# Kernel optimization log

Measured on AMD Instinct MI355X. Metric: run time of the kernel, lower is better.

The kernel has to match this reference:

```python
import jax, jax.numpy as jnp
import numpy as np

N = 8192          # nodes in batch
D_IN = 512        # in_channels
G = 512           # global_dim
D_OUT = 512       # out_channels
H = 8             # heads
C = 2048          # num_centroids
NUM_NODES = 100000


def setup_inputs() -> dict:
    key = jax.random.key(0)
    ks = jax.random.split(key, 10)
    s = lambda fan_in: 1.0 / np.sqrt(fan_in)
    return {
        "x": jax.random.normal(ks[0], (N, D_IN), jnp.float32),
        "W_proj": jax.random.normal(ks[1], (D_IN, G), jnp.float32) * s(D_IN),
        "b_proj": jnp.zeros((G,), jnp.float32),
        "W_q": jax.random.normal(ks[2], (G, D_OUT), jnp.float32) * s(G),
        "b_q": jnp.zeros((D_OUT,), jnp.float32),
        "W_k": jax.random.normal(ks[3], (G, D_OUT), jnp.float32) * s(G),
        "b_k": jnp.zeros((D_OUT,), jnp.float32),
        "W_v": jax.random.normal(ks[4], (G, D_OUT), jnp.float32) * s(G),
        "b_v": jnp.zeros((D_OUT,), jnp.float32),
        "k_buf": jax.random.normal(ks[5], (C, G), jnp.float32),
        "v_buf": jax.random.normal(ks[6], (C, G), jnp.float32),
        "ln_gamma": jnp.ones((D_OUT,), jnp.float32),
        "ln_beta": jnp.zeros((D_OUT,), jnp.float32),
        "c_idx": jax.random.randint(ks[7], (NUM_NODES,), 0, C, jnp.int64 if jax.config.jax_enable_x64 else jnp.int32),
        "node_indices": jax.random.randint(ks[8], (N,), 0, NUM_NODES, jnp.int64 if jax.config.jax_enable_x64 else jnp.int32),
    }


def _layer_norm(y, gamma, beta, eps=1e-5):
    mu = jnp.mean(y, axis=-1, keepdims=True)
    var = jnp.var(y, axis=-1, keepdims=True)
    return (y - mu) * jax.lax.rsqrt(var + eps) * gamma + beta


def reference(x, W_proj, b_proj, W_q, b_q, W_k, b_k, W_v, b_v,
              k_buf, v_buf, ln_gamma, ln_beta, c_idx, node_indices):
    h, d = H, D_OUT
    dh = d // h
    scale = 1.0 / np.sqrt(d)  # source scales by 1/sqrt(out_channels)

    q_x = x @ W_proj + b_proj                      # [N, G]
    k_x = jax.lax.stop_gradient(k_buf)             # detach().clone()
    v_x = jax.lax.stop_gradient(v_buf)

    # n (h d) -> h n d
    q = (q_x @ W_q + b_q).reshape(-1, h, dh).transpose(1, 0, 2)   # [h, N, dh]
    k = (k_x @ W_k + b_k).reshape(-1, h, dh).transpose(1, 0, 2)   # [h, C, dh]
    v = (v_x @ W_v + b_v).reshape(-1, h, dh).transpose(1, 0, 2)   # [h, C, dh]

    dots = jnp.einsum('hnd,hcd->hnc', q, k) * scale               # [h, N, C]

    # log-count centroid bias (unique/bincount over the full c_idx buffer)
    counts = jnp.bincount(c_idx, length=C)                        # [C] int
    dots = dots + jnp.log(counts.astype(dots.dtype))              # log(0)=-inf masks empty centroids

    attn = jax.nn.softmax(dots, axis=-1)                          # [h, N, C]
    out = jnp.einsum('hnc,hcd->hnd', attn, v)                     # [h, N, dh]
    out = out.transpose(1, 0, 2).reshape(-1, d)                   # [N, d]

    return _layer_norm(out, ln_gamma, ln_beta)
```

## Files before the change

### kernel.cpp

```cpp
#include <hip/hip_runtime.h>
#include <math.h>

typedef __bf16 bf16x8 __attribute__((ext_vector_type(8)));
typedef __bf16 bf16x2 __attribute__((ext_vector_type(2)));
typedef float f32x4 __attribute__((ext_vector_type(4)));
typedef float f32x16 __attribute__((ext_vector_type(16)));
typedef unsigned u32x2v __attribute__((ext_vector_type(2)));
typedef unsigned short u16;

#define NQ 8192
#define DMODEL 512
#define NHEAD 8
#define DH 64
#define NC 2048
#define NIDX 100000

__device__ __forceinline__ u16 f2bf(float f) {
    unsigned u = __float_as_uint(f);
    u += 0x7fffu + ((u >> 16) & 1u);
    return (u16)(u >> 16);
}
__device__ __forceinline__ float bf2f(u16 h) {
    return __uint_as_float(((unsigned)h) << 16);
}
__device__ __forceinline__ unsigned pk2(float a, float b) {
    bf16x2 t; t[0] = (__bf16)a; t[1] = (__bf16)b;
    return __builtin_bit_cast(unsigned, t);
}
__device__ __forceinline__ void plswap(unsigned& a, unsigned& b) {
    u32x2v r = __builtin_amdgcn_permlane32_swap(a, b, false, false);
    a = r[0]; b = r[1];
}
__device__ __forceinline__ int soff(int q, int col) {
    return q * 256 + ((((col >> 2) ^ (q & 7)) << 2) | (col & 3));
}

__global__ __launch_bounds__(256) void k_prep2(
    const float* __restrict__ Wp, const float* __restrict__ Wq, const float* __restrict__ Wk,
    const float* __restrict__ Wv, const float* __restrict__ bp, const float* __restrict__ bq_,
    const int* __restrict__ cidx,
    u16* __restrict__ Wp_bf, u16* __restrict__ Wq_t, u16* __restrict__ Wk_t,
    u16* __restrict__ Wv_t, int* __restrict__ counts, float* __restrict__ bcomb)
{
    __shared__ float tile[32][33];
    int bid = blockIdx.x, tid = threadIdx.x;
    if (bid < 256) {
        int e = (bid * 256 + tid) * 4;
        float4 v = *(const float4*)(Wp + e);
        ushort4 o;
        o.x = f2bf(v.x); o.y = f2bf(v.y); o.z = f2bf(v.z); o.w = f2bf(v.w);
        *(ushort4*)(Wp_bf + e) = o;
    } else if (bid < 1024) {
        const float* W; u16* Wt; int tb;
        if (bid < 512)       { W = Wq; Wt = Wq_t; tb = bid - 256; }
        else if (bid < 768)  { W = Wk; Wt = Wk_t; tb = bid - 512; }
        else                 { W = Wv; Wt = Wv_t; tb = bid - 768; }
        int c0 = (tb & 15) * 32, r0 = (tb >> 4) * 32;
        int tx = tid & 31, ty = tid >> 5;
#pragma unroll
        for (int i = 0; i < 4; i++)
            tile[ty + i * 8][tx] = W[(size_t)(r0 + ty + i * 8) * DMODEL + c0 + tx];
        __syncthreads();
#pragma unroll
        for (int i = 0; i < 4; i++)
            Wt[(size_t)(c0 + ty + i * 8) * DMODEL + r0 + tx] = f2bf(tile[tx][ty + i * 8]);
    } else if (bid < 1152) {
        for (int i = (bid - 1024) * 256 + tid; i < NIDX; i += 128 * 256)
            atomicAdd(&counts[cidx[i]], 1);
    } else {
        int j = (bid - 1152) * 256 + tid;
        float s = bq_[j];
        for (int k = 0; k < DMODEL; k++) s += bp[k] * Wq[(size_t)k * DMODEL + j];
        bcomb[j] = s;
    }
}

template <int A_F32, int OUT_T>
__device__ __forceinline__ void gemm_bt_body(
    const void* __restrict__ A_, const u16* __restrict__ Bt,
    const float* __restrict__ bias, u16* __restrict__ Cmat,
    int M, int N, int K, int bx, int by)
{
    constexpr int LDP = 40;
    __shared__ __align__(16) u16 As[128 * LDP];
    __shared__ __align__(16) u16 Bs[128 * LDP];
    int tid = threadIdx.x;
    int lane = tid & 63, wid = tid >> 6;
    int wrow = (wid >> 1) * 64, wcol = (wid & 1) * 64;
    int m0 = by * 128, n0 = bx * 128;
    int lr = lane & 15, lg = lane >> 4;
    f32x4 acc[4][4] = {};

    for (int k0 = 0; k0 < K; k0 += 32) {
#pragma unroll
        for (int c = 0; c < 2; c++) {
            int ch = tid + c * 256;
            int row = ch >> 2, colc = (ch & 3) * 8;
            uint4 av;
            if (A_F32) {
                const float* Af = (const float*)A_;
                float4 a0 = *(const float4*)(Af + (size_t)(m0 + row) * K + k0 + colc);
                float4 a1 = *(const float4*)(Af + (size_t)(m0 + row) * K + k0 + colc + 4);
                av.x = pk2(a0.x, a0.y); av.y = pk2(a0.z, a0.w);
                av.z = pk2(a1.x, a1.y); av.w = pk2(a1.z, a1.w);
            } else {
                av = *(const uint4*)((const u16*)A_ + (size_t)(m0 + row) * K + k0 + colc);
            }
            *(uint4*)(&As[row * LDP + colc]) = av;
            uint4 bv = *(const uint4*)(Bt + (size_t)(n0 + row) * K + k0 + colc);
            *(uint4*)(&Bs[row * LDP + colc]) = bv;
        }
        __syncthreads();
        bf16x8 af[4], bfr[4];
#pragma unroll
        for (int m = 0; m < 4; m++)
            af[m] = *(const bf16x8*)(&As[(wrow + m * 16 + lr) * LDP + lg * 8]);
#pragma unroll
        for (int n = 0; n < 4; n++)
            bfr[n] = *(const bf16x8*)(&Bs[(wcol + n * 16 + lr) * LDP + lg * 8]);
#pragma unroll
        for (int m = 0; m < 4; m++)
#pragma unroll
            for (int n = 0; n < 4; n++)
                acc[m][n] = __builtin_amdgcn_mfma_f32_16x16x32_bf16(af[m], bfr[n], acc[m][n], 0, 0, 0);
        __syncthreads();
    }
#pragma unroll
    for (int n = 0; n < 4; n++) {
        int col = n0 + wcol + n * 16 + lr;
        float bv = bias ? bias[col] : 0.0f;
#pragma unroll
        for (int m = 0; m < 4; m++) {
            int rbase = m0 + wrow + m * 16 + lg * 4;
            if (OUT_T == 1) {
                int hh = col >> 6, T = (col >> 5) & 1, ql = col & 31;
                int t = rbase >> 5, cc = rbase & 31;
                int u = ((cc >> 4) * 2 + ((cc >> 3) & 1)) * 2 + T;
                size_t off = (size_t)hh * 131072 + (size_t)t * 2048 + u * 256 + ql * 8 + (cc & 7);
                ushort4 o4;
                o4.x = f2bf(acc[m][n][0] + bv);
                o4.y = f2bf(acc[m][n][1] + bv);
                o4.z = f2bf(acc[m][n][2] + bv);
                o4.w = f2bf(acc[m][n][3] + bv);
                *(ushort4*)(Cmat + off) = o4;
            } else if (OUT_T == 2) {
                int hh = col >> 6, m2 = (col >> 4) & 3, h2 = (col >> 3) & 1, jj = col & 7;
                size_t ub = (size_t)hh * 131072 + (size_t)(m2 * 2 + h2) * 256 + jj;
#pragma unroll
                for (int r = 0; r < 4; r++) {
                    int c = rbase + r;
                    Cmat[ub + (size_t)(c >> 5) * 2048 + (c & 31) * 8] = f2bf(acc[m][n][r] + bv);
                }
            } else {
#pragma unroll
                for (int r = 0; r < 4; r++)
                    Cmat[(size_t)(rbase + r) * N + col] = f2bf(acc[m][n][r] + bv);
            }
        }
    }
}

__global__ __launch_bounds__(256) void k_gemm_wc(
    const u16* __restrict__ A, const u16* __restrict__ Bt, u16* __restrict__ Cmat)
{
    gemm_bt_body<0, 0>(A, Bt, nullptr, Cmat, DMODEL, DMODEL, DMODEL, blockIdx.x, blockIdx.y);
}

__global__ __launch_bounds__(256) void k_gemm_all(
    const float* __restrict__ kb, const u16* __restrict__ Wkt, const float* __restrict__ bk,
    u16* __restrict__ Kp,
    const float* __restrict__ vb, const u16* __restrict__ Wvt, const float* __restrict__ bv,
    u16* __restrict__ Vp,
    const float* __restrict__ x, const u16* __restrict__ WcombT,
    const float* __restrict__ bcomb, u16* __restrict__ Qm)
{
    int b = blockIdx.x;
    if (b < 64)
        gemm_bt_body<1, 2>(kb, Wkt, bk, Kp, NC, DMODEL, DMODEL, b & 3, b >> 2);
    else if (b < 128)
        gemm_bt_body<1, 1>(vb, Wvt, bv, Vp, NC, DMODEL, DMODEL, (b - 64) & 3, (b - 64) >> 2);
    else
        gemm_bt_body<1, 0>(x, WcombT, bcomb, Qm, NQ, DMODEL, DMODEL, (b - 128) & 3, (b - 128) >> 2);
}

__global__ __launch_bounds__(512, 2) void k_attn8(
    const u16* __restrict__ Q, const u16* __restrict__ Kp, const u16* __restrict__ Vp,
    const int* __restrict__ counts, const float* __restrict__ ln_g,
    const float* __restrict__ ln_b, float* __restrict__ Out, float scale2)
{
    __shared__ float sbias[NC];
    __shared__ unsigned sO[32 * 256];

    int tid = threadIdx.x;
    int lane = tid & 63, wid = tid >> 6;
    int h = wid;
    int ql = lane & 31, hi = lane >> 5;
    int q0 = blockIdx.x * 32;
    int hbase = h * DH;

#pragma unroll
    for (int i = 0; i < 4; i++)
        sbias[tid + i * 512] = log2f((float)counts[tid + i * 512]) - 16.0f;

    bf16x8 qf[4];
#pragma unroll
    for (int m = 0; m < 4; m++)
        qf[m] = *(const bf16x8*)(Q + (size_t)(q0 + ql) * DMODEL + hbase + m * 16 + hi * 8);

    const u16* klane = Kp + (size_t)h * 131072 + hi * 256 + ql * 8;
    const u16* vlane = Vp + (size_t)h * 131072 + hi * 512 + ql * 8;

    bf16x8 kf0[4], kf1[4], vf0[4], vf1[4];
#pragma unroll
    for (int m = 0; m < 4; m++)
        kf0[m] = *(const bf16x8*)(klane + m * 512);
#pragma unroll
    for (int T = 0; T < 2; T++)
#pragma unroll
        for (int ss = 0; ss < 2; ss++)
            vf0[T * 2 + ss] = *(const bf16x8*)(vlane + ss * 1024 + T * 256);

    f32x16 o0 = {}, o1 = {};
    float l_part = 0.f;

    __syncthreads();

    auto body = [&](int t, bf16x8 (&kfc)[4], bf16x8 (&vfc)[4],
                    bf16x8 (&kfn)[4], bf16x8 (&vfn)[4]) {
        const u16* kp = klane + (size_t)(t + 1) * 2048;
        const u16* vp = vlane + (size_t)(t + 1) * 2048;
#pragma unroll
        for (int m = 0; m < 4; m++)
            kfn[m] = *(const bf16x8*)(kp + m * 512);
#pragma unroll
        for (int T = 0; T < 2; T++)
#pragma unroll
            for (int ss = 0; ss < 2; ss++)
                vfn[T * 2 + ss] = *(const bf16x8*)(vp + ss * 1024 + T * 256);

        f32x4 bq[4];
#pragma unroll
        for (int j = 0; j < 4; j++)
            bq[j] = *(const f32x4*)(sbias + t * 32 + 8 * j + 4 * hi);

        f32x16 acc = {};
        __builtin_amdgcn_s_setprio(1);
#pragma unroll
        for (int m = 0; m < 4; m++)
            acc = __builtin_amdgcn_mfma_f32_32x32x16_bf16(kfc[m], qf[m], acc, 0, 0, 0);
        __builtin_amdgcn_s_setprio(0);

        unsigned u[8];
        float rs0 = 0.f, rs1 = 0.f;
#pragma unroll
        for (int j = 0; j < 8; j++) {
            float p0 = exp2f(acc[2 * j] * scale2 + bq[(2 * j) >> 2][(2 * j) & 3]);
            float p1 = exp2f(acc[2 * j + 1] * scale2 + bq[(2 * j + 1) >> 2][(2 * j + 1) & 3]);
            rs0 += p0; rs1 += p1;
            u[j] = pk2(p0, p1);
        }
        l_part += rs0 + rs1;

        plswap(u[0], u[2]); plswap(u[1], u[3]);
        plswap(u[4], u[6]); plswap(u[5], u[7]);
        bf16x8 pb0 = __builtin_bit_cast(bf16x8, *(uint4*)&u[0]);
        bf16x8 pb1 = __builtin_bit_cast(bf16x8, *(uint4*)&u[4]);

        __builtin_amdgcn_s_setprio(1);
        o0 = __builtin_amdgcn_mfma_f32_32x32x16_bf16(vfc[0], pb0, o0, 0, 0, 0);
        o0 = __builtin_amdgcn_mfma_f32_32x32x16_bf16(vfc[1], pb1, o0, 0, 0, 0);
        o1 = __builtin_amdgcn_mfma_f32_32x32x16_bf16(vfc[2], pb0, o1, 0, 0, 0);
        o1 = __builtin_amdgcn_mfma_f32_32x32x16_bf16(vfc[3], pb1, o1, 0, 0, 0);
        __builtin_amdgcn_s_setprio(0);
    };

    for (int t = 0; t < NC / 32; t += 2) {
        body(t,     kf0, vf0, kf1, vf1);
        body(t + 1, kf1, vf1, kf0, vf0);
    }

    float l_tot = l_part + __shfl_xor(l_part, 32);
    float inv = 1.0f / l_tot;

#pragma unroll
    for (int T = 0; T < 2; T++)
#pragma unroll
        for (int j = 0; j < 8; j++) {
            int dw = T * 16 + (j & 1) + 4 * (j >> 1) + 2 * hi;
            float a = (T == 0) ? o0[2 * j] : o1[2 * j];
            float b = (T == 0) ? o0[2 * j + 1] : o1[2 * j + 1];
            sO[soff(ql, h * 32 + dw)] = pk2(a * inv, b * inv);
        }
    __syncthreads();

    float4 g0 = *(const float4*)(ln_g + lane * 8);
    float4 g1 = *(const float4*)(ln_g + lane * 8 + 4);
    float4 b0 = *(const float4*)(ln_b + lane * 8);
    float4 b1 = *(const float4*)(ln_b + lane * 8 + 4);
#pragma unroll
    for (int rr = 0; rr < 4; rr++) {
        int r = wid * 4 + rr;
        uint4 pw = *(const uint4*)(&sO[r * 256 + ((lane ^ (r & 7)) << 2)]);
        float v[8];
        v[0] = bf2f((u16)(pw.x & 0xffff)); v[1] = bf2f((u16)(pw.x >> 16));
        v[2] = bf2f((u16)(pw.y & 0xffff)); v[3] = bf2f((u16)(pw.y >> 16));
        v[4] = bf2f((u16)(pw.z & 0xffff)); v[5] = bf2f((u16)(pw.z >> 16));
        v[6] = bf2f((u16)(pw.w & 0xffff)); v[7] = bf2f((u16)(pw.w >> 16));
        float sum = 0.f, sq = 0.f;
#pragma unroll
        for (int j = 0; j < 8; j++) { sum += v[j]; sq += v[j] * v[j]; }
#pragma unroll
        for (int msk = 1; msk <= 32; msk <<= 1) { sum += __shfl_xor(sum, msk); sq += __shfl_xor(sq, msk); }
        float mu = sum * (1.f / DMODEL);
        float var = sq * (1.f / DMODEL) - mu * mu;
        float rstd = rsqrtf(var + 1e-5f);
        float o[8];
        o[0] = (v[0] - mu) * rstd * g0.x + b0.x; o[1] = (v[1] - mu) * rstd * g0.y + b0.y;
        o[2] = (v[2] - mu) * rstd * g0.z + b0.z; o[3] = (v[3] - mu) * rstd * g0.w + b0.w;
        o[4] = (v[4] - mu) * rstd * g1.x + b1.x; o[5] = (v[5] - mu) * rstd * g1.y + b1.y;
        o[6] = (v[6] - mu) * rstd * g1.z + b1.z; o[7] = (v[7] - mu) * rstd * g1.w + b1.w;
        float* op = Out + (size_t)(q0 + r) * DMODEL + lane * 8;
        *(float4*)op = *(float4*)&o[0];
        *(float4*)(op + 4) = *(float4*)&o[4];
    }
}

extern "C" void kernel_launch(void* const* d_in, const int* in_sizes, int n_in,
                              void* d_out, int out_size, void* d_ws, size_t ws_size,
                              hipStream_t stream)
{
    const float* x      = (const float*)d_in[0];
    const float* W_proj = (const float*)d_in[1];
    const float* b_proj = (const float*)d_in[2];
    const float* W_q    = (const float*)d_in[3];
    const float* b_q    = (const float*)d_in[4];
    const float* W_k    = (const float*)d_in[5];
    const float* b_k    = (const float*)d_in[6];
    const float* W_v    = (const float*)d_in[7];
    const float* b_v    = (const float*)d_in[8];
    const float* k_buf  = (const float*)d_in[9];
    const float* v_buf  = (const float*)d_in[10];
    const float* ln_g   = (const float*)d_in[11];
    const float* ln_b   = (const float*)d_in[12];
    const int*   c_idx  = (const int*)d_in[13];
    float* out = (float*)d_out;

    char* ws = (char*)d_ws;
    size_t off = 0;
    auto alloc = [&](size_t bytes) -> void* {
        void* p = ws + off;
        off += (bytes + 255) & ~(size_t)255;
        return p;
    };
    u16* Wp_bf  = (u16*)alloc((size_t)DMODEL * DMODEL * 2);
    u16* Wq_t   = (u16*)alloc((size_t)DMODEL * DMODEL * 2);
    u16* Wk_t   = (u16*)alloc((size_t)DMODEL * DMODEL * 2);
    u16* Wv_t   = (u16*)alloc((size_t)DMODEL * DMODEL * 2);
    u16* WcombT = (u16*)alloc((size_t)DMODEL * DMODEL * 2);
    u16* Qm     = (u16*)alloc((size_t)NQ * DMODEL * 2);
    u16* Kpm    = (u16*)alloc((size_t)NC * DMODEL * 2);
    u16* Vpm    = (u16*)alloc((size_t)DMODEL * NC * 2);
    int*   counts = (int*)alloc(NC * 4);
    float* bcomb  = (float*)alloc(DMODEL * 4);
    (void)alloc(262144);

    hipMemsetAsync(counts, 0, NC * 4, stream);

    k_prep2<<<dim3(1154), dim3(256), 0, stream>>>(
        W_proj, W_q, W_k, W_v, b_proj, b_q, c_idx,
        Wp_bf, Wq_t, Wk_t, Wv_t, counts, bcomb);

    k_gemm_wc<<<dim3(4, 4), dim3(256), 0, stream>>>(Wq_t, Wp_bf, WcombT);

    k_gemm_all<<<dim3(384), dim3(256), 0, stream>>>(
        k_buf, Wk_t, b_k, Kpm,
        v_buf, Wv_t, b_v, Vpm,
        x, WcombT, bcomb, Qm);

    k_attn8<<<dim3(NQ / 32), dim3(512), 0, stream>>>(Qm, Kpm, Vpm, counts, ln_g, ln_b, out, 0.06375872f);
    (void)in_sizes; (void)n_in; (void)out_size; (void)ws_size;
}
```

Baseline: 136.8 us.

## Fold combined-weight GEMM into prep kernel and move bincount into projection launch

Removes the separate k_gemm_wc launch. The prep kernel now computes W_comb directly from fp32 W_q (read transposed) and W_proj, which drops the Wp_bf and Wq_t intermediate buffers. The centroid bincount moves into extra blocks of the projection GEMM kernel, and in the attention loop the next K/V fragment loads are placed after the MFMAs that consume the current ones. The aim is to cut one kernel launch and some memory traffic; the cost is strided scalar fp32 loads in the W_comb GEMM and possible changes to register pressure and latency hiding in attention.

Result: faster. 124.9 us (-8.7%).

```diff
diff --git a/kernel.cpp b/kernel.cpp
--- a/kernel.cpp
+++ b/kernel.cpp
@@ -35,49 +35,9 @@
     return q * 256 + ((((col >> 2) ^ (q & 7)) << 2) | (col & 3));
 }
 
-__global__ __launch_bounds__(256) void k_prep2(
-    const float* __restrict__ Wp, const float* __restrict__ Wq, const float* __restrict__ Wk,
-    const float* __restrict__ Wv, const float* __restrict__ bp, const float* __restrict__ bq_,
-    const int* __restrict__ cidx,
-    u16* __restrict__ Wp_bf, u16* __restrict__ Wq_t, u16* __restrict__ Wk_t,
-    u16* __restrict__ Wv_t, int* __restrict__ counts, float* __restrict__ bcomb)
-{
-    __shared__ float tile[32][33];
-    int bid = blockIdx.x, tid = threadIdx.x;
-    if (bid < 256) {
-        int e = (bid * 256 + tid) * 4;
-        float4 v = *(const float4*)(Wp + e);
-        ushort4 o;
-        o.x = f2bf(v.x); o.y = f2bf(v.y); o.z = f2bf(v.z); o.w = f2bf(v.w);
-        *(ushort4*)(Wp_bf + e) = o;
-    } else if (bid < 1024) {
-        const float* W; u16* Wt; int tb;
-        if (bid < 512)       { W = Wq; Wt = Wq_t; tb = bid - 256; }
-        else if (bid < 768)  { W = Wk; Wt = Wk_t; tb = bid - 512; }
-        else                 { W = Wv; Wt = Wv_t; tb = bid - 768; }
-        int c0 = (tb & 15) * 32, r0 = (tb >> 4) * 32;
-        int tx = tid & 31, ty = tid >> 5;
-#pragma unroll
-        for (int i = 0; i < 4; i++)
-            tile[ty + i * 8][tx] = W[(size_t)(r0 + ty + i * 8) * DMODEL + c0 + tx];
-        __syncthreads();
-#pragma unroll
-        for (int i = 0; i < 4; i++)
-            Wt[(size_t)(c0 + ty + i * 8) * DMODEL + r0 + tx] = f2bf(tile[tx][ty + i * 8]);
-    } else if (bid < 1152) {
-        for (int i = (bid - 1024) * 256 + tid; i < NIDX; i += 128 * 256)
-            atomicAdd(&counts[cidx[i]], 1);
-    } else {
-        int j = (bid - 1152) * 256 + tid;
-        float s = bq_[j];
-        for (int k = 0; k < DMODEL; k++) s += bp[k] * Wq[(size_t)k * DMODEL + j];
-        bcomb[j] = s;
-    }
-}
-
-template <int A_F32, int OUT_T>
+template <int A_MODE, int B_MODE, int OUT_T>
 __device__ __forceinline__ void gemm_bt_body(
-    const void* __restrict__ A_, const u16* __restrict__ Bt,
+    const void* __restrict__ A_, const void* __restrict__ Bt_,
     const float* __restrict__ bias, u16* __restrict__ Cmat,
     int M, int N, int K, int bx, int by)
 {
@@ -97,17 +57,34 @@
             int ch = tid + c * 256;
             int row = ch >> 2, colc = (ch & 3) * 8;
             uint4 av;
-            if (A_F32) {
+            if (A_MODE == 1) {
                 const float* Af = (const float*)A_;
                 float4 a0 = *(const float4*)(Af + (size_t)(m0 + row) * K + k0 + colc);
                 float4 a1 = *(const float4*)(Af + (size_t)(m0 + row) * K + k0 + colc + 4);
                 av.x = pk2(a0.x, a0.y); av.y = pk2(a0.z, a0.w);
                 av.z = pk2(a1.x, a1.y); av.w = pk2(a1.z, a1.w);
+            } else if (A_MODE == 2) {
+                const float* Af = (const float*)A_;
+                float e[8];
+#pragma unroll
+                for (int i = 0; i < 8; i++)
+                    e[i] = Af[(size_t)(k0 + colc + i) * M + m0 + row];
+                av.x = pk2(e[0], e[1]); av.y = pk2(e[2], e[3]);
+                av.z = pk2(e[4], e[5]); av.w = pk2(e[6], e[7]);
             } else {
                 av = *(const uint4*)((const u16*)A_ + (size_t)(m0 + row) * K + k0 + colc);
             }
             *(uint4*)(&As[row * LDP + colc]) = av;
-            uint4 bv = *(const uint4*)(Bt + (size_t)(n0 + row) * K + k0 + colc);
+            uint4 bv;
+            if (B_MODE == 1) {
+                const float* Bf = (const float*)Bt_;
+                float4 b0 = *(const float4*)(Bf + (size_t)(n0 + row) * K + k0 + colc);
+                float4 b1 = *(const float4*)(Bf + (size_t)(n0 + row) * K + k0 + colc + 4);
+                bv.x = pk2(b0.x, b0.y); bv.y = pk2(b0.z, b0.w);
+                bv.z = pk2(b1.x, b1.y); bv.w = pk2(b1.z, b1.w);
+            } else {
+                bv = *(const uint4*)((const u16*)Bt_ + (size_t)(n0 + row) * K + k0 + colc);
+            }
             *(uint4*)(&Bs[row * LDP + colc]) = bv;
         }
         __syncthreads();
@@ -160,10 +137,36 @@
     }
 }
 
-__global__ __launch_bounds__(256) void k_gemm_wc(
-    const u16* __restrict__ A, const u16* __restrict__ Bt, u16* __restrict__ Cmat)
-{
-    gemm_bt_body<0, 0>(A, Bt, nullptr, Cmat, DMODEL, DMODEL, DMODEL, blockIdx.x, blockIdx.y);
+__global__ __launch_bounds__(256) void k_prep2(
+    const float* __restrict__ Wq, const float* __restrict__ Wk, const float* __restrict__ Wv,
+    const float* __restrict__ Wp, const float* __restrict__ bp, const float* __restrict__ bq_,
+    u16* __restrict__ Wk_t, u16* __restrict__ Wv_t,
+    u16* __restrict__ WcombT, float* __restrict__ bcomb)
+{
+    __shared__ float tile[32][33];
+    int bid = blockIdx.x, tid = threadIdx.x;
+    if (bid < 16) {
+        gemm_bt_body<2, 1, 0>(Wq, Wp, nullptr, WcombT, DMODEL, DMODEL, DMODEL,
+                              bid & 3, bid >> 2);
+    } else if (bid < 18) {
+        int j = (bid - 16) * 256 + tid;
+        float s = bq_[j];
+        for (int k = 0; k < DMODEL; k++) s += bp[k] * Wq[(size_t)k * DMODEL + j];
+        bcomb[j] = s;
+    } else {
+        const float* W; u16* Wt; int tb;
+        if (bid < 274) { W = Wk; Wt = Wk_t; tb = bid - 18; }
+        else           { W = Wv; Wt = Wv_t; tb = bid - 274; }
+        int c0 = (tb & 15) * 32, r0 = (tb >> 4) * 32;
+        int tx = tid & 31, ty = tid >> 5;
+#pragma unroll
+        for (int i = 0; i < 4; i++)
+            tile[ty + i * 8][tx] = W[(size_t)(r0 + ty + i * 8) * DMODEL + c0 + tx];
+        __syncthreads();
+#pragma unroll
+        for (int i = 0; i < 4; i++)
+            Wt[(size_t)(c0 + ty + i * 8) * DMODEL + r0 + tx] = f2bf(tile[tx][ty + i * 8]);
+    }
 }
 
 __global__ __launch_bounds__(256) void k_gemm_all(
@@ -172,15 +175,20 @@
     const float* __restrict__ vb, const u16* __restrict__ Wvt, const float* __restrict__ bv,
     u16* __restrict__ Vp,
     const float* __restrict__ x, const u16* __restrict__ WcombT,
-    const float* __restrict__ bcomb, u16* __restrict__ Qm)
+    const float* __restrict__ bcomb, u16* __restrict__ Qm,
+    const int* __restrict__ cidx, int* __restrict__ counts)
 {
     int b = blockIdx.x;
     if (b < 64)
-        gemm_bt_body<1, 2>(kb, Wkt, bk, Kp, NC, DMODEL, DMODEL, b & 3, b >> 2);
+        gemm_bt_body<1, 0, 2>(kb, Wkt, bk, Kp, NC, DMODEL, DMODEL, b & 3, b >> 2);
     else if (b < 128)
-        gemm_bt_body<1, 1>(vb, Wvt, bv, Vp, NC, DMODEL, DMODEL, (b - 64) & 3, (b - 64) >> 2);
-    else
-        gemm_bt_body<1, 0>(x, WcombT, bcomb, Qm, NQ, DMODEL, DMODEL, (b - 128) & 3, (b - 128) >> 2);
+        gemm_bt_body<1, 0, 1>(vb, Wvt, bv, Vp, NC, DMODEL, DMODEL, (b - 64) & 3, (b - 64) >> 2);
+    else if (b < 384)
+        gemm_bt_body<1, 0, 0>(x, WcombT, bcomb, Qm, NQ, DMODEL, DMODEL, (b - 128) & 3, (b - 128) >> 2);
+    else {
+        for (int i = (b - 384) * 256 + threadIdx.x; i < NIDX; i += 128 * 256)
+            atomicAdd(&counts[cidx[i]], 1);
+    }
 }
 
 __global__ __launch_bounds__(512, 2) void k_attn8(
@@ -227,17 +235,6 @@
 
     auto body = [&](int t, bf16x8 (&kfc)[4], bf16x8 (&vfc)[4],
                     bf16x8 (&kfn)[4], bf16x8 (&vfn)[4]) {
-        const u16* kp = klane + (size_t)(t + 1) * 2048;
-        const u16* vp = vlane + (size_t)(t + 1) * 2048;
-#pragma unroll
-        for (int m = 0; m < 4; m++)
-            kfn[m] = *(const bf16x8*)(kp + m * 512);
-#pragma unroll
-        for (int T = 0; T < 2; T++)
-#pragma unroll
-            for (int ss = 0; ss < 2; ss++)
-                vfn[T * 2 + ss] = *(const bf16x8*)(vp + ss * 1024 + T * 256);
-
         f32x4 bq[4];
 #pragma unroll
         for (int j = 0; j < 4; j++)
@@ -249,6 +246,11 @@
         for (int m = 0; m < 4; m++)
             acc = __builtin_amdgcn_mfma_f32_32x32x16_bf16(kfc[m], qf[m], acc, 0, 0, 0);
         __builtin_amdgcn_s_setprio(0);
+
+        const u16* kp = klane + (size_t)(t + 1) * 2048;
+#pragma unroll
+        for (int m = 0; m < 4; m++)
+            kfn[m] = *(const bf16x8*)(kp + m * 512);
 
         unsigned u[8];
         float rs0 = 0.f, rs1 = 0.f;
@@ -272,6 +274,13 @@
         o1 = __builtin_amdgcn_mfma_f32_32x32x16_bf16(vfc[2], pb0, o1, 0, 0, 0);
         o1 = __builtin_amdgcn_mfma_f32_32x32x16_bf16(vfc[3], pb1, o1, 0, 0, 0);
         __builtin_amdgcn_s_setprio(0);
+
+        const u16* vp = vlane + (size_t)(t + 1) * 2048;
+#pragma unroll
+        for (int T = 0; T < 2; T++)
+#pragma unroll
+            for (int ss = 0; ss < 2; ss++)
+                vfn[T * 2 + ss] = *(const bf16x8*)(vp + ss * 1024 + T * 256);
     };
 
     for (int t = 0; t < NC / 32; t += 2) {
@@ -352,8 +361,6 @@
         off += (bytes + 255) & ~(size_t)255;
         return p;
     };
-    u16* Wp_bf  = (u16*)alloc((size_t)DMODEL * DMODEL * 2);
-    u16* Wq_t   = (u16*)alloc((size_t)DMODEL * DMODEL * 2);
     u16* Wk_t   = (u16*)alloc((size_t)DMODEL * DMODEL * 2);
     u16* Wv_t   = (u16*)alloc((size_t)DMODEL * DMODEL * 2);
     u16* WcombT = (u16*)alloc((size_t)DMODEL * DMODEL * 2);
@@ -362,20 +369,19 @@
     u16* Vpm    = (u16*)alloc((size_t)DMODEL * NC * 2);
     int*   counts = (int*)alloc(NC * 4);
     float* bcomb  = (float*)alloc(DMODEL * 4);
-    (void)alloc(262144);
+    (void)alloc(2200000);
 
     hipMemsetAsync(counts, 0, NC * 4, stream);
 
-    k_prep2<<<dim3(1154), dim3(256), 0, stream>>>(
-        W_proj, W_q, W_k, W_v, b_proj, b_q, c_idx,
-        Wp_bf, Wq_t, Wk_t, Wv_t, counts, bcomb);
-
-    k_gemm_wc<<<dim3(4, 4), dim3(256), 0, stream>>>(Wq_t, Wp_bf, WcombT);
-
-    k_gemm_all<<<dim3(384), dim3(256), 0, stream>>>(
+    k_prep2<<<dim3(530), dim3(256), 0, stream>>>(
+        W_q, W_k, W_v, W_proj, b_proj, b_q,
+        Wk_t, Wv_t, WcombT, bcomb);
+
+    k_gemm_all<<<dim3(512), dim3(256), 0, stream>>>(
         k_buf, Wk_t, b_k, Kpm,
         v_buf, Wv_t, b_v, Vpm,
-        x, WcombT, bcomb, Qm);
+        x, WcombT, bcomb, Qm,
+        c_idx, counts);
 
     k_attn8<<<dim3(NQ / 32), dim3(512), 0, stream>>>(Qm, Kpm, Vpm, counts, ln_g, ln_b, out, 0.06375872f);
     (void)in_sizes; (void)n_in; (void)out_size; (void)ws_size;
```
